# Kernel tuning notes

Measured on AMD Instinct MI355X. Metric: run time of the kernel, lower is better.

Reference implementation:

```python
import jax, jax.numpy as jnp
import numpy as np

N_NODES = 20000


def _segment_softmax(alpha, dst, num_nodes):
    # numerically-stable softmax over edges grouped by destination node
    m = jax.ops.segment_max(alpha, dst, num_segments=num_nodes)
    m = jnp.where(jnp.isfinite(m), m, 0.0)
    a = jnp.exp(alpha - m[dst])
    denom = jax.ops.segment_sum(a, dst, num_segments=num_nodes)
    return a / denom[dst]


def mgcn_conv(x, src, dst, edge_type, basis, att, weight, root, bias, num_nodes):
    # x: [N, in], basis: [B, in, out], att: [R, B], weight: [R, out=in]
    x_i = x[dst]                                   # [E, in] target feats
    x_j = x[src]                                   # [E, in] source feats
    # per-edge attention logit: sum_d x_i[d] * w_r[d] * x_j[d]
    alpha = jnp.sum(x_i * weight[edge_type] * x_j, axis=1)   # [E]
    alpha = _segment_softmax(alpha, dst, num_nodes)          # [E]
    # basis-decomposed per-edge transform: x_j @ (att_r . basis)
    t = jnp.einsum('ei,bio->ebo', x_j, basis)                # [E, B, out]
    msg = jnp.einsum('ebo,eb->eo', t, att[edge_type])        # [E, out]
    msg = msg * alpha[:, None]
    out = jax.ops.segment_sum(msg, dst, num_segments=num_nodes)  # [N, out]
    return out + x @ root + bias


def setup_inputs() -> dict:
    key = jax.random.key(0)
    ks = jax.random.split(key, 16)
    E, D, R, B, N = 32768, 128, 474, 64, N_NODES
    s = 0.05
    return {
        'entity': jnp.arange(N, dtype=jnp.int64) if jax.config.jax_enable_x64 else jnp.arange(N, dtype=jnp.int32),
        'edge_index': jax.random.randint(ks[0], (2, E), 0, N, dtype=jnp.int32),
        'edge_type': jax.random.randint(ks[1], (E,), 0, R, dtype=jnp.int32),
        'emb_table': jax.random.normal(ks[2], (N, D), dtype=jnp.float32),
        'basis1': jax.random.normal(ks[3], (B, D, D), dtype=jnp.float32) * s,
        'att1': jax.random.normal(ks[4], (R, B), dtype=jnp.float32) * s,
        'weight1': jax.random.normal(ks[5], (R, D), dtype=jnp.float32) * s,
        'root1': jax.random.normal(ks[6], (D, D), dtype=jnp.float32) * s,
        'bias1': jnp.zeros((D,), dtype=jnp.float32),
        'basis2': jax.random.normal(ks[7], (B, D, D), dtype=jnp.float32) * s,
        'att2': jax.random.normal(ks[8], (R, B), dtype=jnp.float32) * s,
        'weight2': jax.random.normal(ks[9], (R, D), dtype=jnp.float32) * s,
        'root2': jax.random.normal(ks[10], (D, D), dtype=jnp.float32) * s,
        'bias2': jnp.zeros((D,), dtype=jnp.float32),
    }


def reference(entity, edge_index, edge_type, emb_table,
              basis1, att1, weight1, root1, bias1,
              basis2, att2, weight2, root2, bias2):
    src, dst = edge_index[0], edge_index[1]   # PyG: (source j, target i)
    x = emb_table[entity]                     # embedding lookup
    h = jax.nn.relu(mgcn_conv(x, src, dst, edge_type, basis1, att1,
                              weight1, root1, bias1, N_NODES))
    # dropout is identity at inference
    out = mgcn_conv(h, src, dst, edge_type, basis2, att2,
                    weight2, root2, bias2, N_NODES)
    return out
```

## Files before the change

### kernel.cpp

```cpp
#include <hip/hip_runtime.h>
#include <hip/hip_bf16.h>

#define N_NODES 20000
#define N_EDGES 32768
#define DIM 128
#define N_REL 474
#define N_BASIS 64
#define TILE_E 64
#define MAXCH (N_EDGES / TILE_E + N_REL)
#define WSTRIDE 260
#define HIST_BLKS 16
#define EDGES_PER_HIST (N_EDGES / HIST_BLKS)

typedef __bf16 bf16x8 __attribute__((ext_vector_type(8)));
typedef float f32x4 __attribute__((ext_vector_type(4)));

__device__ __forceinline__ unsigned short f2b(float f) {
    unsigned u = __float_as_uint(f);
    unsigned r = (u + 0x7FFFu + ((u >> 16) & 1u)) >> 16;
    return (unsigned short)r;
}
__device__ __forceinline__ float b2f(unsigned short s) {
    return __uint_as_float(((unsigned)s) << 16);
}
__device__ __forceinline__ __bf16 u2b(unsigned short u) {
    union { unsigned short u; __bf16 b; } c; c.u = u; return c.b;
}

__global__ __launch_bounds__(256) void prepmix_kernel(const float4* __restrict__ emb,
                                                      const int* __restrict__ entity,
                                                      const int* __restrict__ etype,
                                                      ushort4* __restrict__ xb4,
                                                      float4* __restrict__ zreg, int zcount4,
                                                      int* __restrict__ partial,
                                                      const float* __restrict__ att1,
                                                      const float* __restrict__ basis1,
                                                      unsigned short* __restrict__ W1,
                                                      const float* __restrict__ att2,
                                                      const float* __restrict__ basis2,
                                                      unsigned short* __restrict__ W2) {
    __shared__ __align__(16) unsigned short bt[64 * WSTRIDE];
    int t = threadIdx.x;
    if (blockIdx.x < 1024) {
        int wi = blockIdx.x;
        const float* att   = (wi >= 512) ? att2 : att1;
        const float* basis = (wi >= 512) ? basis2 : basis1;
        unsigned short* W  = (wi >= 512) ? W2 : W1;
        int io0 = (wi & 63) * 256;
        int r0 = ((wi >> 6) & 7) * 64;
#pragma unroll
        for (int p = 0; p < 16; p++) {
            int c = t + 256 * p;
            int k = c >> 6, of = c & 63;
            float4 v = *(const float4*)(basis + (size_t)k * (DIM * DIM) + io0 + of * 4);
            ushort4 s;
            s.x = f2b(v.x); s.y = f2b(v.y); s.z = f2b(v.z); s.w = f2b(v.w);
            *(ushort4*)&bt[k * WSTRIDE + of * 4] = s;
        }
        __syncthreads();

        int w = t >> 6, l = t & 63, n = l & 15, q = l >> 4;
        f32x4 acc[4][4] = {};
#pragma unroll
        for (int kb = 0; kb < 2; kb++) {
            int kbase = kb * 32 + q * 8;
            bf16x8 a[4];
#pragma unroll
            for (int rt = 0; rt < 4; rt++) {
                int rm = min(r0 + rt * 16 + n, N_REL - 1);
                const float* ap = att + (size_t)rm * N_BASIS + kbase;
#pragma unroll
                for (int j = 0; j < 8; j++) a[rt][j] = u2b(f2b(ap[j]));
            }
#pragma unroll
            for (int c = 0; c < 4; c++) {
                int ob = w * 64 + c * 16 + n;
                bf16x8 b;
#pragma unroll
                for (int j = 0; j < 8; j++) b[j] = u2b(bt[(kbase + j) * WSTRIDE + ob]);
#pragma unroll
                for (int rt = 0; rt < 4; rt++)
                    acc[rt][c] = __builtin_amdgcn_mfma_f32_16x16x32_bf16(a[rt], b, acc[rt][c], 0, 0, 0);
            }
        }
#pragma unroll
        for (int rt = 0; rt < 4; rt++) {
#pragma unroll
            for (int c = 0; c < 4; c++) {
                int col = io0 + w * 64 + c * 16 + n;
#pragma unroll
                for (int rg = 0; rg < 4; rg++) {
                    int r = r0 + rt * 16 + q * 4 + rg;
                    if (r < N_REL) W[(size_t)r * (DIM * DIM) + col] = f2b(acc[rt][c][rg]);
                }
            }
        }
    } else {
        int pb = blockIdx.x - 1024;
        int gtid = pb * 256 + t;
        int gsz = 1024 * 256;
        int total4 = N_NODES * DIM / 4;
        for (int i = gtid; i < total4; i += gsz) {
            int n = i >> 5, rem = i & 31;
            float4 v = emb[(size_t)entity[n] * 32 + rem];
            ushort4 s;
            s.x = f2b(v.x); s.y = f2b(v.y); s.z = f2b(v.z); s.w = f2b(v.w);
            xb4[i] = s;
        }
        float4 z = make_float4(0.f, 0.f, 0.f, 0.f);
        for (int i = gtid; i < zcount4; i += gsz) zreg[i] = z;
        if (pb < HIST_BLKS) {
            int* ih = (int*)bt;
            for (int i = t; i < N_REL; i += 256) ih[i] = 0;
            __syncthreads();
            int e0 = pb * EDGES_PER_HIST;
            for (int e = e0 + t; e < e0 + EDGES_PER_HIST; e += 256)
                atomicAdd(&ih[etype[e]], 1);
            __syncthreads();
            for (int i = t; i < N_REL; i += 256) partial[pb * N_REL + i] = ih[i];
        }
    }
}

__global__ void scanr_kernel(const int* __restrict__ partial, int* __restrict__ offs,
                             int* __restrict__ cursor, int* __restrict__ chunk_r,
                             int* __restrict__ chunk_o, int* __restrict__ nchunks) {
    __shared__ int s[512];
    __shared__ int lnc;
    int t = threadIdx.x;
    int v = 0;
    if (t < N_REL) {
#pragma unroll
        for (int k = 0; k < HIST_BLKS; k++) v += partial[k * N_REL + t];
    }
    s[t] = v;
    if (t == 0) lnc = 0;
    __syncthreads();
    for (int d = 1; d < 512; d <<= 1) {
        int add = (t >= d) ? s[t - d] : 0;
        __syncthreads();
        s[t] += add;
        __syncthreads();
    }
    int excl = s[t] - v;
    if (t < N_REL) { offs[t] = excl; cursor[t] = excl; }
    if (t == 0) offs[N_REL] = N_EDGES;
    if (t < N_REL && v > 0) {
        int nc = (v + TILE_E - 1) / TILE_E;
        int cb = atomicAdd(&lnc, nc);
        for (int c = 0; c < nc; c++) { chunk_r[cb + c] = t; chunk_o[cb + c] = excl + c * TILE_E; }
    }
    __syncthreads();
    if (t == 0) *nchunks = lnc;
}

__global__ __launch_bounds__(256) void scatlogit_kernel(const unsigned short* __restrict__ xb,
                                                        const float* __restrict__ w,
                                                        const int* __restrict__ src,
                                                        const int* __restrict__ dst,
                                                        const int* __restrict__ et,
                                                        int* __restrict__ cursor,
                                                        int* __restrict__ eids,
                                                        float* __restrict__ alpha,
                                                        float* __restrict__ den, int E) {
    int wid = (blockIdx.x * 256 + threadIdx.x) >> 6;
    int lane = threadIdx.x & 63;
    if (wid >= E) return;
    int s = src[wid], d = dst[wid], r = et[wid];
    if (lane == 0) {
        int p = atomicAdd(&cursor[r], 1);
        eids[p] = wid;
    }
    unsigned ax = ((const unsigned*)(xb + (size_t)s * DIM))[lane];
    unsigned bx = ((const unsigned*)(xb + (size_t)d * DIM))[lane];
    float2 wv = ((const float2*)(w + (size_t)r * DIM))[lane];
    float v = b2f((unsigned short)(ax & 0xFFFF)) * wv.x * b2f((unsigned short)(bx & 0xFFFF))
            + b2f((unsigned short)(ax >> 16)) * wv.y * b2f((unsigned short)(bx >> 16));
    for (int off = 32; off > 0; off >>= 1) v += __shfl_xor(v, off, 64);
    if (lane == 0) {
        float a = expf(v);
        alpha[wid] = a;
        atomicAdd(&den[d], a);
    }
}

__global__ __launch_bounds__(256) void logitexp_kernel(const unsigned short* __restrict__ xb,
                                                       const float* __restrict__ w,
                                                       const int* __restrict__ src,
                                                       const int* __restrict__ dst,
                                                       const int* __restrict__ et,
                                                       float* __restrict__ alpha,
                                                       float* __restrict__ den, int E) {
    int wid = (blockIdx.x * 256 + threadIdx.x) >> 6;
    int lane = threadIdx.x & 63;
    if (wid >= E) return;
    int s = src[wid], d = dst[wid], r = et[wid];
    unsigned ax = ((const unsigned*)(xb + (size_t)s * DIM))[lane];
    unsigned bx = ((const unsigned*)(xb + (size_t)d * DIM))[lane];
    float2 wv = ((const float2*)(w + (size_t)r * DIM))[lane];
    float v = b2f((unsigned short)(ax & 0xFFFF)) * wv.x * b2f((unsigned short)(bx & 0xFFFF))
            + b2f((unsigned short)(ax >> 16)) * wv.y * b2f((unsigned short)(bx >> 16));
    for (int off = 32; off > 0; off >>= 1) v += __shfl_xor(v, off, 64);
    if (lane == 0) {
        float a = expf(v);
        alpha[wid] = a;
        atomicAdd(&den[d], a);
    }
}

__global__ __launch_bounds__(256) void msg_kernel(const unsigned short* __restrict__ xb,
                                                  const unsigned short* __restrict__ W,
                                                  const int* __restrict__ chunk_r,
                                                  const int* __restrict__ chunk_off,
                                                  const int* __restrict__ nchunks,
                                                  const int* __restrict__ eids,
                                                  const int* __restrict__ offs,
                                                  const int* __restrict__ src,
                                                  const int* __restrict__ dst,
                                                  const float* __restrict__ ae,
                                                  const float* __restrict__ denom,
                                                  float* __restrict__ outacc) {
    if ((int)blockIdx.x >= *nchunks) return;
    int r = chunk_r[blockIdx.x];
    int base = chunk_off[blockIdx.x];
    int nE = min(TILE_E, offs[r + 1] - base);
    const unsigned short* Wr = W + (size_t)r * (DIM * DIM);

    __shared__ unsigned short wt[128 * 136];
    __shared__ unsigned short xjf[8192];
    __shared__ float scf[TILE_E];
    __shared__ int sdd[TILE_E];

    int t = threadIdx.x;
    if (t < TILE_E) {
        if (t < nE) {
            int e = eids[base + t];
            int d_ = dst[e];
            sdd[t] = d_;
            scf[t] = ae[e] / denom[d_];
        } else { sdd[t] = 0; scf[t] = 0.f; }
    }
#pragma unroll
    for (int p = 0; p < 4; p++) {
        int c = t + 256 * p;
        int g = c >> 6;
        int rt = g >> 2, kb = g & 3;
        int q = (c >> 4) & 3, m = c & 15;
        int e = rt * 16 + m;
        int oct = kb * 4 + q;
        int4 v = make_int4(0, 0, 0, 0);
        if (e < nE)
            v = *(const int4*)(xb + (size_t)src[eids[base + e]] * DIM + oct * 8);
        *(int4*)&xjf[c * 8] = v;
    }
#pragma unroll
    for (int p = 0; p < 8; p++) {
        int c = t + 256 * p;
        int k = c >> 4, oct = c & 15;
        int4 v = *(const int4*)(Wr + k * DIM + oct * 8);
        *(int4*)&wt[k * 136 + oct * 8] = v;
    }
    __syncthreads();

    int w = t >> 6, l = t & 63, n = l & 15, q = l >> 4;
    f32x4 acc[2][4] = {};
#pragma unroll
    for (int kb = 0; kb < 4; kb++) {
        bf16x8 a[4];
#pragma unroll
        for (int rt = 0; rt < 4; rt++) a[rt] = *(const bf16x8*)&xjf[((rt * 4 + kb) * 64 + l) * 8];
        int kbase = kb * 32 + q * 8;
#pragma unroll
        for (int c = 0; c < 2; c++) {
            int ob = (w * 2 + c) * 16 + n;
            bf16x8 b;
#pragma unroll
            for (int j = 0; j < 8; j++) b[j] = u2b(wt[(kbase + j) * 136 + ob]);
#pragma unroll
            for (int rt = 0; rt < 4; rt++)
                acc[c][rt] = __builtin_amdgcn_mfma_f32_16x16x32_bf16(a[rt], b, acc[c][rt], 0, 0, 0);
        }
    }
#pragma unroll
    for (int c = 0; c < 2; c++) {
        int col = (w * 2 + c) * 16 + n;
#pragma unroll
        for (int rt = 0; rt < 4; rt++) {
#pragma unroll
            for (int rg = 0; rg < 4; rg++) {
                int e = rt * 16 + q * 4 + rg;
                if (e < nE)
                    atomicAdd(&outacc[(size_t)sdd[e] * DIM + col], scf[e] * acc[c][rt][rg]);
            }
        }
    }
}

__global__ __launch_bounds__(256) void root_kernel(const unsigned short* __restrict__ xb,
                                                   const float* __restrict__ rootM,
                                                   const float* __restrict__ bias,
                                                   const float* __restrict__ accbuf,
                                                   unsigned short* __restrict__ outb,
                                                   float* __restrict__ outf,
                                                   int mode, int N) {
    int n0 = blockIdx.x * 64;
    __shared__ unsigned short wt[128 * 136];
    __shared__ unsigned short xrf[8192];
    int t = threadIdx.x;
#pragma unroll
    for (int p = 0; p < 4; p++) {
        int c = t + 256 * p;
        int g = c >> 6;
        int rt = g >> 2, kb = g & 3;
        int q = (c >> 4) & 3, m = c & 15;
        int row = n0 + rt * 16 + m;
        int oct = kb * 4 + q;
        int4 v = make_int4(0, 0, 0, 0);
        if (row < N) v = *(const int4*)(xb + (size_t)row * DIM + oct * 8);
        *(int4*)&xrf[c * 8] = v;
    }
#pragma unroll
    for (int p = 0; p < 16; p++) {
        int c = t + 256 * p;
        int k = c >> 5, of = c & 31;
        float4 v = *(const float4*)(rootM + k * DIM + of * 4);
        ushort4 s;
        s.x = f2b(v.x); s.y = f2b(v.y); s.z = f2b(v.z); s.w = f2b(v.w);
        *(ushort4*)&wt[k * 136 + of * 4] = s;
    }
    __syncthreads();

    int w = t >> 6, l = t & 63, n = l & 15, q = l >> 4;
    f32x4 acc[2][4] = {};
#pragma unroll
    for (int kb = 0; kb < 4; kb++) {
        bf16x8 a[4];
#pragma unroll
        for (int rt = 0; rt < 4; rt++) a[rt] = *(const bf16x8*)&xrf[((rt * 4 + kb) * 64 + l) * 8];
        int kbase = kb * 32 + q * 8;
#pragma unroll
        for (int c = 0; c < 2; c++) {
            int ob = (w * 2 + c) * 16 + n;
            bf16x8 b;
#pragma unroll
            for (int j = 0; j < 8; j++) b[j] = u2b(wt[(kbase + j) * 136 + ob]);
#pragma unroll
            for (int rt = 0; rt < 4; rt++)
                acc[c][rt] = __builtin_amdgcn_mfma_f32_16x16x32_bf16(a[rt], b, acc[c][rt], 0, 0, 0);
        }
    }
#pragma unroll
    for (int c = 0; c < 2; c++) {
        int col = (w * 2 + c) * 16 + n;
        float bo = bias[col];
#pragma unroll
        for (int rt = 0; rt < 4; rt++) {
#pragma unroll
            for (int rg = 0; rg < 4; rg++) {
                int row = n0 + rt * 16 + q * 4 + rg;
                if (row < N) {
                    float v = accbuf[(size_t)row * DIM + col] + acc[c][rt][rg] + bo;
                    if (mode) {
                        outb[(size_t)row * DIM + col] = f2b(fmaxf(v, 0.f));
                    } else {
                        outf[(size_t)row * DIM + col] = v;
                    }
                }
            }
        }
    }
}

extern "C" void kernel_launch(void* const* d_in, const int* in_sizes, int n_in,
                              void* d_out, int out_size, void* d_ws, size_t ws_size,
                              hipStream_t stream) {
    const int N = N_NODES, E = N_EDGES, R = N_REL;

    const int* entity = (const int*)d_in[0];
    const int* eidx   = (const int*)d_in[1];
    const int* src    = eidx;
    const int* dst    = eidx + E;
    const int* etype  = (const int*)d_in[2];
    const float* emb  = (const float*)d_in[3];
    const float* basis1 = (const float*)d_in[4];
    const float* att1   = (const float*)d_in[5];
    const float* w1     = (const float*)d_in[6];
    const float* root1  = (const float*)d_in[7];
    const float* bias1  = (const float*)d_in[8];
    const float* basis2 = (const float*)d_in[9];
    const float* att2   = (const float*)d_in[10];
    const float* w2     = (const float*)d_in[11];
    const float* root2  = (const float*)d_in[12];
    const float* bias2  = (const float*)d_in[13];
    float* out = (float*)d_out;

    size_t off = 0;
    auto alloc = [&](size_t bytes) -> void* {
        void* p = (char*)d_ws + off;
        off += (bytes + 255) & ~(size_t)255;
        return p;
    };
    unsigned short* W1 = (unsigned short*)alloc((size_t)R * DIM * DIM * 2);
    unsigned short* W2 = (unsigned short*)alloc((size_t)R * DIM * DIM * 2);
    unsigned short* xb = (unsigned short*)alloc((size_t)N * DIM * 2);
    unsigned short* hb = (unsigned short*)alloc((size_t)N * DIM * 2);
    float* zreg   = (float*)alloc((size_t)(2 * N * DIM + 2 * N) * 4);
    float* acc1   = zreg;
    float* acc2   = zreg + (size_t)N * DIM;
    float* denom1 = zreg + (size_t)2 * N * DIM;
    float* denom2 = denom1 + N;
    float* alpha  = (float*)alloc((size_t)E * 4);
    int* partial  = (int*)alloc((size_t)HIST_BLKS * R * 4);
    int* nchunks  = (int*)alloc(256);
    int* offs     = (int*)alloc((size_t)(R + 1) * 4);
    int* cursor   = (int*)alloc((size_t)R * 4);
    int* eids     = (int*)alloc((size_t)E * 4);
    int* chunk_r  = (int*)alloc((size_t)MAXCH * 4);
    int* chunk_o  = (int*)alloc((size_t)MAXCH * 4);

    int zcount4 = (2 * N * DIM + 2 * N) / 4;

    prepmix_kernel<<<2048, 256, 0, stream>>>((const float4*)emb, entity, etype,
                                             (ushort4*)xb, (float4*)zreg, zcount4, partial,
                                             att1, basis1, W1, att2, basis2, W2);
    scanr_kernel<<<1, 512, 0, stream>>>(partial, offs, cursor, chunk_r, chunk_o, nchunks);

    scatlogit_kernel<<<E / 4, 256, 0, stream>>>(xb, w1, src, dst, etype, cursor, eids,
                                                alpha, denom1, E);
    msg_kernel<<<MAXCH, 256, 0, stream>>>(xb, W1, chunk_r, chunk_o, nchunks,
                                          eids, offs, src, dst, alpha, denom1, acc1);
    root_kernel<<<(N + 63) / 64, 256, 0, stream>>>(xb, root1, bias1, acc1, hb, nullptr, 1, N);

    logitexp_kernel<<<E / 4, 256, 0, stream>>>(hb, w2, src, dst, etype, alpha, denom2, E);
    msg_kernel<<<MAXCH, 256, 0, stream>>>(hb, W2, chunk_r, chunk_o, nchunks,
                                          eids, offs, src, dst, alpha, denom2, acc2);
    root_kernel<<<(N + 63) / 64, 256, 0, stream>>>(hb, root2, bias2, acc2, nullptr, out, 0, N);
}
```

Measured before the change: 230.9 us.

## Fuse root GEMM into logit kernel and seed accumulators with root output

The root transform (x @ root + bias) now runs as extra blocks of the logit kernel and writes straight into the message accumulator (or the final output), so the big accumulator no longer has to be zero-filled. The message kernel then atomically adds into that pre-seeded buffer, and a small relu/cast kernel produces the bf16 hidden layer. This drops the separate root kernels, the large memset and the read-back of the accumulator. In exchange, the root blocks read the root matrix from global memory and convert it to bf16 per element instead of staging it in LDS, and the second layer's atomics now land directly on the output.

```diff
diff --git a/kernel.cpp b/kernel.cpp
--- a/kernel.cpp
+++ b/kernel.cpp
@@ -11,6 +11,8 @@
 #define WSTRIDE 260
 #define HIST_BLKS 16
 #define EDGES_PER_HIST (N_EDGES / HIST_BLKS)
+#define LOGIT_BLKS (N_EDGES / 4)
+#define ROOT_BLKS ((N_NODES + 63) / 64)
 
 typedef __bf16 bf16x8 __attribute__((ext_vector_type(8)));
 typedef float f32x4 __attribute__((ext_vector_type(4)));
@@ -154,57 +156,89 @@
     if (t == 0) *nchunks = lnc;
 }
 
-__global__ __launch_bounds__(256) void scatlogit_kernel(const unsigned short* __restrict__ xb,
-                                                        const float* __restrict__ w,
-                                                        const int* __restrict__ src,
-                                                        const int* __restrict__ dst,
-                                                        const int* __restrict__ et,
-                                                        int* __restrict__ cursor,
-                                                        int* __restrict__ eids,
-                                                        float* __restrict__ alpha,
-                                                        float* __restrict__ den, int E) {
-    int wid = (blockIdx.x * 256 + threadIdx.x) >> 6;
-    int lane = threadIdx.x & 63;
-    if (wid >= E) return;
-    int s = src[wid], d = dst[wid], r = et[wid];
-    if (lane == 0) {
-        int p = atomicAdd(&cursor[r], 1);
-        eids[p] = wid;
-    }
-    unsigned ax = ((const unsigned*)(xb + (size_t)s * DIM))[lane];
-    unsigned bx = ((const unsigned*)(xb + (size_t)d * DIM))[lane];
-    float2 wv = ((const float2*)(w + (size_t)r * DIM))[lane];
-    float v = b2f((unsigned short)(ax & 0xFFFF)) * wv.x * b2f((unsigned short)(bx & 0xFFFF))
-            + b2f((unsigned short)(ax >> 16)) * wv.y * b2f((unsigned short)(bx >> 16));
-    for (int off = 32; off > 0; off >>= 1) v += __shfl_xor(v, off, 64);
-    if (lane == 0) {
-        float a = expf(v);
-        alpha[wid] = a;
-        atomicAdd(&den[d], a);
-    }
-}
-
-__global__ __launch_bounds__(256) void logitexp_kernel(const unsigned short* __restrict__ xb,
-                                                       const float* __restrict__ w,
-                                                       const int* __restrict__ src,
-                                                       const int* __restrict__ dst,
-                                                       const int* __restrict__ et,
-                                                       float* __restrict__ alpha,
-                                                       float* __restrict__ den, int E) {
-    int wid = (blockIdx.x * 256 + threadIdx.x) >> 6;
-    int lane = threadIdx.x & 63;
-    if (wid >= E) return;
-    int s = src[wid], d = dst[wid], r = et[wid];
-    unsigned ax = ((const unsigned*)(xb + (size_t)s * DIM))[lane];
-    unsigned bx = ((const unsigned*)(xb + (size_t)d * DIM))[lane];
-    float2 wv = ((const float2*)(w + (size_t)r * DIM))[lane];
-    float v = b2f((unsigned short)(ax & 0xFFFF)) * wv.x * b2f((unsigned short)(bx & 0xFFFF))
-            + b2f((unsigned short)(ax >> 16)) * wv.y * b2f((unsigned short)(bx >> 16));
-    for (int off = 32; off > 0; off >>= 1) v += __shfl_xor(v, off, 64);
-    if (lane == 0) {
-        float a = expf(v);
-        alpha[wid] = a;
-        atomicAdd(&den[d], a);
+__global__ __launch_bounds__(256) void fused_kernel(const unsigned short* __restrict__ xb,
+                                                    const float* __restrict__ w,
+                                                    const int* __restrict__ src,
+                                                    const int* __restrict__ dst,
+                                                    const int* __restrict__ et,
+                                                    int* __restrict__ cursor,
+                                                    int* __restrict__ eids,
+                                                    int do_scatter,
+                                                    float* __restrict__ alpha,
+                                                    float* __restrict__ den,
+                                                    const float* __restrict__ rootM,
+                                                    const float* __restrict__ bias,
+                                                    float* __restrict__ target) {
+    __shared__ __align__(16) unsigned short xrf[8192];
+    int t = threadIdx.x;
+    if (blockIdx.x < LOGIT_BLKS) {
+        int wid = (blockIdx.x * 256 + t) >> 6;
+        int lane = t & 63;
+        int s = src[wid], d = dst[wid], r = et[wid];
+        if (do_scatter && lane == 0) {
+            int p = atomicAdd(&cursor[r], 1);
+            eids[p] = wid;
+        }
+        unsigned ax = ((const unsigned*)(xb + (size_t)s * DIM))[lane];
+        unsigned bx = ((const unsigned*)(xb + (size_t)d * DIM))[lane];
+        float2 wv = ((const float2*)(w + (size_t)r * DIM))[lane];
+        float v = b2f((unsigned short)(ax & 0xFFFF)) * wv.x * b2f((unsigned short)(bx & 0xFFFF))
+                + b2f((unsigned short)(ax >> 16)) * wv.y * b2f((unsigned short)(bx >> 16));
+        for (int off = 32; off > 0; off >>= 1) v += __shfl_xor(v, off, 64);
+        if (lane == 0) {
+            float a = expf(v);
+            alpha[wid] = a;
+            atomicAdd(&den[d], a);
+        }
+    } else {
+        int n0 = (blockIdx.x - LOGIT_BLKS) * 64;
+#pragma unroll
+        for (int p = 0; p < 4; p++) {
+            int c = t + 256 * p;
+            int g = c >> 6;
+            int rt = g >> 2, kb = g & 3;
+            int q = (c >> 4) & 3, m = c & 15;
+            int row = n0 + rt * 16 + m;
+            int oct = kb * 4 + q;
+            int4 v = make_int4(0, 0, 0, 0);
+            if (row < N_NODES) v = *(const int4*)(xb + (size_t)row * DIM + oct * 8);
+            *(int4*)&xrf[c * 8] = v;
+        }
+        __syncthreads();
+
+        int w_ = t >> 6, l = t & 63, n = l & 15, q = l >> 4;
+        f32x4 acc[2][4] = {};
+#pragma unroll
+        for (int kb = 0; kb < 4; kb++) {
+            bf16x8 a[4];
+#pragma unroll
+            for (int rt = 0; rt < 4; rt++) a[rt] = *(const bf16x8*)&xrf[((rt * 4 + kb) * 64 + l) * 8];
+            int kbase = kb * 32 + q * 8;
+#pragma unroll
+            for (int c = 0; c < 2; c++) {
+                int col = (w_ * 2 + c) * 16 + n;
+                bf16x8 b;
+#pragma unroll
+                for (int j = 0; j < 8; j++) b[j] = u2b(f2b(rootM[(kbase + j) * DIM + col]));
+#pragma unroll
+                for (int rt = 0; rt < 4; rt++)
+                    acc[c][rt] = __builtin_amdgcn_mfma_f32_16x16x32_bf16(a[rt], b, acc[c][rt], 0, 0, 0);
+            }
+        }
+#pragma unroll
+        for (int c = 0; c < 2; c++) {
+            int col = (w_ * 2 + c) * 16 + n;
+            float bo = bias[col];
+#pragma unroll
+            for (int rt = 0; rt < 4; rt++) {
+#pragma unroll
+                for (int rg = 0; rg < 4; rg++) {
+                    int row = n0 + rt * 16 + q * 4 + rg;
+                    if (row < N_NODES)
+                        target[(size_t)row * DIM + col] = acc[c][rt][rg] + bo;
+                }
+            }
+        }
     }
 }
 
@@ -296,79 +330,16 @@
     }
 }
 
-__global__ __launch_bounds__(256) void root_kernel(const unsigned short* __restrict__ xb,
-                                                   const float* __restrict__ rootM,
-                                                   const float* __restrict__ bias,
-                                                   const float* __restrict__ accbuf,
-                                                   unsigned short* __restrict__ outb,
-                                                   float* __restrict__ outf,
-                                                   int mode, int N) {
-    int n0 = blockIdx.x * 64;
-    __shared__ unsigned short wt[128 * 136];
-    __shared__ unsigned short xrf[8192];
-    int t = threadIdx.x;
-#pragma unroll
-    for (int p = 0; p < 4; p++) {
-        int c = t + 256 * p;
-        int g = c >> 6;
-        int rt = g >> 2, kb = g & 3;
-        int q = (c >> 4) & 3, m = c & 15;
-        int row = n0 + rt * 16 + m;
-        int oct = kb * 4 + q;
-        int4 v = make_int4(0, 0, 0, 0);
-        if (row < N) v = *(const int4*)(xb + (size_t)row * DIM + oct * 8);
-        *(int4*)&xrf[c * 8] = v;
-    }
-#pragma unroll
-    for (int p = 0; p < 16; p++) {
-        int c = t + 256 * p;
-        int k = c >> 5, of = c & 31;
-        float4 v = *(const float4*)(rootM + k * DIM + of * 4);
-        ushort4 s;
-        s.x = f2b(v.x); s.y = f2b(v.y); s.z = f2b(v.z); s.w = f2b(v.w);
-        *(ushort4*)&wt[k * 136 + of * 4] = s;
-    }
-    __syncthreads();
-
-    int w = t >> 6, l = t & 63, n = l & 15, q = l >> 4;
-    f32x4 acc[2][4] = {};
-#pragma unroll
-    for (int kb = 0; kb < 4; kb++) {
-        bf16x8 a[4];
-#pragma unroll
-        for (int rt = 0; rt < 4; rt++) a[rt] = *(const bf16x8*)&xrf[((rt * 4 + kb) * 64 + l) * 8];
-        int kbase = kb * 32 + q * 8;
-#pragma unroll
-        for (int c = 0; c < 2; c++) {
-            int ob = (w * 2 + c) * 16 + n;
-            bf16x8 b;
-#pragma unroll
-            for (int j = 0; j < 8; j++) b[j] = u2b(wt[(kbase + j) * 136 + ob]);
-#pragma unroll
-            for (int rt = 0; rt < 4; rt++)
-                acc[c][rt] = __builtin_amdgcn_mfma_f32_16x16x32_bf16(a[rt], b, acc[c][rt], 0, 0, 0);
-        }
-    }
-#pragma unroll
-    for (int c = 0; c < 2; c++) {
-        int col = (w * 2 + c) * 16 + n;
-        float bo = bias[col];
-#pragma unroll
-        for (int rt = 0; rt < 4; rt++) {
-#pragma unroll
-            for (int rg = 0; rg < 4; rg++) {
-                int row = n0 + rt * 16 + q * 4 + rg;
-                if (row < N) {
-                    float v = accbuf[(size_t)row * DIM + col] + acc[c][rt][rg] + bo;
-                    if (mode) {
-                        outb[(size_t)row * DIM + col] = f2b(fmaxf(v, 0.f));
-                    } else {
-                        outf[(size_t)row * DIM + col] = v;
-                    }
-                }
-            }
-        }
-    }
+__global__ __launch_bounds__(256) void relucast_kernel(const float4* __restrict__ acc,
+                                                       ushort4* __restrict__ hb) {
+    int i = blockIdx.x * 256 + threadIdx.x;
+    float4 v = acc[i];
+    ushort4 s;
+    s.x = f2b(fmaxf(v.x, 0.f));
+    s.y = f2b(fmaxf(v.y, 0.f));
+    s.z = f2b(fmaxf(v.z, 0.f));
+    s.w = f2b(fmaxf(v.w, 0.f));
+    hb[i] = s;
 }
 
 extern "C" void kernel_launch(void* const* d_in, const int* in_sizes, int n_in,
@@ -404,11 +375,10 @@
     unsigned short* W2 = (unsigned short*)alloc((size_t)R * DIM * DIM * 2);
     unsigned short* xb = (unsigned short*)alloc((size_t)N * DIM * 2);
     unsigned short* hb = (unsigned short*)alloc((size_t)N * DIM * 2);
-    float* zreg   = (float*)alloc((size_t)(2 * N * DIM + 2 * N) * 4);
-    float* acc1   = zreg;
-    float* acc2   = zreg + (size_t)N * DIM;
-    float* denom1 = zreg + (size_t)2 * N * DIM;
-    float* denom2 = denom1 + N;
+    float* acc1   = (float*)alloc((size_t)N * DIM * 4);
+    float* zreg   = (float*)alloc((size_t)2 * N * 4);
+    float* denom1 = zreg;
+    float* denom2 = zreg + N;
     float* alpha  = (float*)alloc((size_t)E * 4);
     int* partial  = (int*)alloc((size_t)HIST_BLKS * R * 4);
     int* nchunks  = (int*)alloc(256);
@@ -418,21 +388,21 @@
     int* chunk_r  = (int*)alloc((size_t)MAXCH * 4);
     int* chunk_o  = (int*)alloc((size_t)MAXCH * 4);
 
-    int zcount4 = (2 * N * DIM + 2 * N) / 4;
+    int zcount4 = 2 * N / 4;
 
     prepmix_kernel<<<2048, 256, 0, stream>>>((const float4*)emb, entity, etype,
                                              (ushort4*)xb, (float4*)zreg, zcount4, partial,
                                              att1, basis1, W1, att2, basis2, W2);
     scanr_kernel<<<1, 512, 0, stream>>>(partial, offs, cursor, chunk_r, chunk_o, nchunks);
 
-    scatlogit_kernel<<<E / 4, 256, 0, stream>>>(xb, w1, src, dst, etype, cursor, eids,
-                                                alpha, denom1, E);
+    fused_kernel<<<LOGIT_BLKS + ROOT_BLKS, 256, 0, stream>>>(
+        xb, w1, src, dst, etype, cursor, eids, 1, alpha, denom1, root1, bias1, acc1);
     msg_kernel<<<MAXCH, 256, 0, stream>>>(xb, W1, chunk_r, chunk_o, nchunks,
                                           eids, offs, src, dst, alpha, denom1, acc1);
-    root_kernel<<<(N + 63) / 64, 256, 0, stream>>>(xb, root1, bias1, acc1, hb, nullptr, 1, N);
-
-    logitexp_kernel<<<E / 4, 256, 0, stream>>>(hb, w2, src, dst, etype, alpha, denom2, E);
+    relucast_kernel<<<N * DIM / 4 / 256, 256, 0, stream>>>((const float4*)acc1, (ushort4*)hb);
+
+    fused_kernel<<<LOGIT_BLKS + ROOT_BLKS, 256, 0, stream>>>(
+        hb, w2, src, dst, etype, cursor, eids, 0, alpha, denom2, root2, bias2, out);
     msg_kernel<<<MAXCH, 256, 0, stream>>>(hb, W2, chunk_r, chunk_o, nchunks,
-                                          eids, offs, src, dst, alpha, denom2, acc2);
-    root_kernel<<<(N + 63) / 64, 256, 0, stream>>>(hb, root2, bias2, acc2, nullptr, out, 0, N);
-}
+                                          eids, offs, src, dst, alpha, denom2, out);
+}
```

Result: faster. 225.5 us (-2.3%).
